# Optimization experiments

Measured on AMD Instinct MI355X. Metric: run time of the kernel, lower is better.

## Reference

```python
import jax, jax.numpy as jnp
import numpy as np

NUM_EMBEDDINGS = 1024
EMBEDDING_DIM = 64
COMMITMENT_COST = 0.25


def setup_inputs() -> dict:
    key = jax.random.key(0)
    k_in, k_cb = jax.random.split(key)
    inputs = jax.random.normal(k_in, (32, 4096, EMBEDDING_DIM), dtype=jnp.float32)
    # matches reset_embeddings(): uniform(-1/num_embeddings, 1/num_embeddings)
    bound = 1.0 / NUM_EMBEDDINGS
    codebook = jax.random.uniform(k_cb, (NUM_EMBEDDINGS, EMBEDDING_DIM),
                                  dtype=jnp.float32, minval=-bound, maxval=bound)
    return {"inputs": inputs, "codebook": codebook}


def reference(inputs, codebook):
    input_shape = inputs.shape
    D = codebook.shape[1]
    x = inputs.reshape(-1, D)  # [N, D]
    # Squared euclidean distances; argmin is invariant to the sqrt used by torch.cdist.
    # dist2[n,k] = ||x_n||^2 - 2 x_n . e_k + ||e_k||^2
    dist2 = (jnp.sum(x * x, axis=1, keepdims=True)
             - 2.0 * (x @ codebook.T)
             + jnp.sum(codebook * codebook, axis=1))  # [N, K]
    encoding_indices = jnp.argmin(dist2, axis=1)  # [N]
    quantized = codebook[encoding_indices].reshape(input_shape)
    loss = (jnp.mean((jax.lax.stop_gradient(quantized) - inputs) ** 2)
            + COMMITMENT_COST * jnp.mean((quantized - jax.lax.stop_gradient(inputs)) ** 2))
    # straight-through estimator
    quantized_st = inputs + jax.lax.stop_gradient(quantized - inputs)
    return quantized_st, loss
```

## Files before the change

### kernel.cpp

```cpp
#include <hip/hip_runtime.h>


typedef __attribute__((ext_vector_type(8))) short short8;
typedef __attribute__((ext_vector_type(4))) float f32x4;

#define VQ_D 64
#define MTILE 512
#define CSTRIDE 68

__device__ inline unsigned short f2bf(float f) {
  union { float f; unsigned u; } v; v.f = f;
  unsigned r = v.u + 0x7FFFu + ((v.u >> 16) & 1u);
  return (unsigned short)(r >> 16);
}

__global__ __launch_bounds__(256) void vq_prep(const float* __restrict__ cb,
                                               float* __restrict__ c2b,
                                               unsigned short* __restrict__ cbb,
                                               float* __restrict__ sse,
                                               unsigned* __restrict__ counter, int K) {
  if (blockIdx.x == 0 && threadIdx.x == 0) { *sse = 0.f; *counter = 0u; }
  int w = (int)((blockIdx.x * 256 + threadIdx.x) >> 6);
  int lane = threadIdx.x & 63;
  if (w >= K) return;
  float v = cb[(size_t)w * VQ_D + lane];
  cbb[(size_t)w * VQ_D + lane] = f2bf(v);
  float s = v * v;
#pragma unroll
  for (int off = 32; off; off >>= 1) s += __shfl_down(s, off);
  if (lane == 0) c2b[w] = s + 0.5f;
}

__global__ __launch_bounds__(512) void vq_main(
    const float* __restrict__ x, const float* __restrict__ cb,
    const float* __restrict__ c2b, const unsigned short* __restrict__ cbb,
    float* __restrict__ out, float* __restrict__ sse_out,
    unsigned* __restrict__ counter, int nblocks) {
  __shared__ unsigned short cbs[1024 * CSTRIDE];
  __shared__ float c2s[1024];
  __shared__ int idxs[MTILE];
  __shared__ float redbuf[8];

  const int tid = threadIdx.x;
  const int wave = tid >> 6;
  const int lane = tid & 63;
  const int quad = lane >> 4;
  const int col = lane & 15;
  const long blockRow0 = (long)blockIdx.x * MTILE;
  const int waveRow0 = wave * 64;

#pragma unroll
  for (int r = 0; r < 16; ++r) {
    int id = r * 512 + tid;
    int code = id >> 3;
    int piece = id & 7;
    short8 v = *(const short8*)(cbb + (size_t)code * VQ_D + piece * 8);
    *(short8*)(cbs + code * CSTRIDE + piece * 8) = v;
  }
  c2s[tid] = c2b[tid];
  c2s[tid + 512] = c2b[tid + 512];

  short8 Af[4][2];
#pragma unroll
  for (int mi = 0; mi < 4; ++mi) {
#pragma unroll
    for (int ks = 0; ks < 2; ++ks) {
      long row = blockRow0 + waveRow0 + mi * 16 + col;
      const f32x4* xp = (const f32x4*)(x + row * VQ_D + ks * 32 + quad * 8);
      f32x4 lo = xp[0];
      f32x4 hi = xp[1];
      short8 a;
      a[0] = (short)f2bf(-2.f * lo[0]); a[1] = (short)f2bf(-2.f * lo[1]);
      a[2] = (short)f2bf(-2.f * lo[2]); a[3] = (short)f2bf(-2.f * lo[3]);
      a[4] = (short)f2bf(-2.f * hi[0]); a[5] = (short)f2bf(-2.f * hi[1]);
      a[6] = (short)f2bf(-2.f * hi[2]); a[7] = (short)f2bf(-2.f * hi[3]);
      Af[mi][ks] = a;
    }
  }

  unsigned bk[4][4];
#pragma unroll
  for (int mi = 0; mi < 4; ++mi)
#pragma unroll
    for (int r = 0; r < 4; ++r) bk[mi][r] = 0xFFFFFFFFu;

  __syncthreads();

  const unsigned short* bbase = cbs + (size_t)col * CSTRIDE + quad * 8;
#pragma unroll 4
  for (int t = 0; t < 64; ++t) {
    const unsigned short* bp = bbase + t * 16 * CSTRIDE;
    short8 b0 = *(const short8*)bp;
    short8 b1 = *(const short8*)(bp + 32);
    float cc = c2s[t * 16 + col];

    f32x4 acc[4];
#pragma unroll
    for (int mi = 0; mi < 4; ++mi) {
      f32x4 a = {cc, cc, cc, cc};
      a = __builtin_amdgcn_mfma_f32_16x16x32_bf16(Af[mi][0], b0, a, 0, 0, 0);
      a = __builtin_amdgcn_mfma_f32_16x16x32_bf16(Af[mi][1], b1, a, 0, 0, 0);
      acc[mi] = a;
    }

    const unsigned code = (unsigned)((t << 4) + col);
#pragma unroll
    for (int mi = 0; mi < 4; ++mi)
#pragma unroll
      for (int r = 0; r < 4; ++r)
        bk[mi][r] = min(bk[mi][r], (__float_as_uint(acc[mi][r]) & 0xFFFFFC00u) | code);
  }

#pragma unroll
  for (int off = 1; off < 16; off <<= 1) {
#pragma unroll
    for (int mi = 0; mi < 4; ++mi)
#pragma unroll
      for (int r = 0; r < 4; ++r) {
        unsigned o = (unsigned)__shfl_xor((int)bk[mi][r], off);
        bk[mi][r] = min(bk[mi][r], o);
      }
  }
  if (col == 0) {
#pragma unroll
    for (int mi = 0; mi < 4; ++mi)
#pragma unroll
      for (int r = 0; r < 4; ++r)
        idxs[waveRow0 + mi * 16 + quad * 4 + r] = (int)(bk[mi][r] & 1023u);
  }
  __syncthreads();

  float sse = 0.f;
  const f32x4* cb4 = (const f32x4*)cb;
  const f32x4* x4 = (const f32x4*)x;
  f32x4* out4 = (f32x4*)out;
#pragma unroll
  for (int i = 0; i < 16; ++i) {
    int f = i * 512 + tid;
    int row_l = f >> 4;
    int d4 = f & 15;
    int idx = idxs[row_l];
    f32x4 cv = cb4[(size_t)idx * 16 + d4];
    long gi = (blockRow0 + row_l) * 16 + d4;
    f32x4 xv = x4[gi];
    out4[gi] = cv;
    f32x4 dv = cv - xv;
    sse += dv[0] * dv[0] + dv[1] * dv[1] + dv[2] * dv[2] + dv[3] * dv[3];
  }
#pragma unroll
  for (int off = 32; off; off >>= 1) sse += __shfl_down(sse, off);
  if (lane == 0) redbuf[wave] = sse;
  __syncthreads();

  if (tid == 0) {
    float s = 0.f;
#pragma unroll
    for (int w = 0; w < 8; ++w) s += redbuf[w];
    atomicAdd(sse_out, s);
    __threadfence();
    unsigned old = atomicAdd(counter, 1u);
    if (old == (unsigned)(nblocks - 1)) {
      float tot = atomicAdd(sse_out, 0.f);
      long nelem = (long)nblocks * MTILE * VQ_D;
      out[nelem] = 1.25f * tot / (float)nelem;
    }
  }
}

extern "C" void kernel_launch(void* const* d_in, const int* in_sizes, int n_in,
                              void* d_out, int out_size, void* d_ws, size_t ws_size,
                              hipStream_t stream) {
  const float* x = (const float*)d_in[0];
  const float* cb = (const float*)d_in[1];
  float* out = (float*)d_out;

  const long n_elem = (long)in_sizes[0];
  const int nrows = (int)(n_elem / VQ_D);
  const int K = in_sizes[1] / VQ_D;
  const int nblocks = nrows / MTILE;

  char* ws = (char*)d_ws;
  float* sse = (float*)ws;
  unsigned* counter = (unsigned*)(ws + 64);
  float* c2b = (float*)(ws + 256);
  unsigned short* cbb = (unsigned short*)(ws + 8192);

  vq_prep<<<dim3((K * 64 + 255) / 256), dim3(256), 0, stream>>>(cb, c2b, cbb, sse, counter, K);
  vq_main<<<dim3(nblocks), dim3(512), 0, stream>>>(x, cb, c2b, cbb, out, sse, counter, nblocks);
}
```

Before: 131.7 us.

## Keep codebook slices in registers and stream input rows through LDS

Each wave now holds a 128-code slice of the bf16 codebook in registers and loops over all 8 row groups of the block. Those rows are staged once as bf16 in a smaller LDS buffer, with the next group's operands prefetched. Per-row argmin keys are merged across waves with LDS atomicMin instead of one wave owning each row. This drops the 139KB codebook LDS copy, which should allow more blocks per CU and remove per-iteration LDS reads of B. The costs are higher register pressure, LDS atomics, and more shuffle reductions (8 rounds instead of one).

```diff
diff --git a/kernel.cpp b/kernel.cpp
--- a/kernel.cpp
+++ b/kernel.cpp
@@ -6,7 +6,8 @@
 
 #define VQ_D 64
 #define MTILE 512
-#define CSTRIDE 68
+#define NTH 512
+#define AS 68
 
 __device__ inline unsigned short f2bf(float f) {
   union { float f; unsigned u; } v; v.f = f;
@@ -31,14 +32,24 @@
   if (lane == 0) c2b[w] = s + 0.5f;
 }
 
-__global__ __launch_bounds__(512) void vq_main(
+#define LOADA(DST, G)                                                                  \
+  {                                                                                    \
+    const int g_ = (G);                                                                \
+    _Pragma("unroll") for (int mi_ = 0; mi_ < 4; ++mi_) {                              \
+      _Pragma("unroll") for (int ks_ = 0; ks_ < 2; ++ks_) {                            \
+        DST[mi_][ks_] = *(const short8*)(xb + (g_ * 64 + mi_ * 16 + col) * AS +        \
+                                         ks_ * 32 + quad * 8);                         \
+      }                                                                                \
+    }                                                                                  \
+  }
+
+__global__ __launch_bounds__(NTH) void vq_main(
     const float* __restrict__ x, const float* __restrict__ cb,
     const float* __restrict__ c2b, const unsigned short* __restrict__ cbb,
     float* __restrict__ out, float* __restrict__ sse_out,
     unsigned* __restrict__ counter, int nblocks) {
-  __shared__ unsigned short cbs[1024 * CSTRIDE];
-  __shared__ float c2s[1024];
-  __shared__ int idxs[MTILE];
+  __shared__ unsigned short xb[MTILE * AS];
+  __shared__ unsigned keys[MTILE];
   __shared__ float redbuf[8];
 
   const int tid = threadIdx.x;
@@ -47,86 +58,85 @@
   const int quad = lane >> 4;
   const int col = lane & 15;
   const long blockRow0 = (long)blockIdx.x * MTILE;
-  const int waveRow0 = wave * 64;
-
-#pragma unroll
-  for (int r = 0; r < 16; ++r) {
-    int id = r * 512 + tid;
-    int code = id >> 3;
+
+  short8 B[8][2];
+  float cc[8];
+  const int code0 = wave * 128;
+#pragma unroll
+  for (int ci = 0; ci < 8; ++ci) {
+    const unsigned short* bp = cbb + (size_t)(code0 + ci * 16 + col) * VQ_D + quad * 8;
+    B[ci][0] = *(const short8*)bp;
+    B[ci][1] = *(const short8*)(bp + 32);
+    cc[ci] = c2b[code0 + ci * 16 + col];
+  }
+
+  keys[tid] = 0xFFFFFFFFu;
+
+#pragma unroll
+  for (int i = 0; i < 8; ++i) {
+    int id = i * NTH + tid;
+    int row = id >> 3;
     int piece = id & 7;
-    short8 v = *(const short8*)(cbb + (size_t)code * VQ_D + piece * 8);
-    *(short8*)(cbs + code * CSTRIDE + piece * 8) = v;
-  }
-  c2s[tid] = c2b[tid];
-  c2s[tid + 512] = c2b[tid + 512];
-
-  short8 Af[4][2];
-#pragma unroll
-  for (int mi = 0; mi < 4; ++mi) {
-#pragma unroll
-    for (int ks = 0; ks < 2; ++ks) {
-      long row = blockRow0 + waveRow0 + mi * 16 + col;
-      const f32x4* xp = (const f32x4*)(x + row * VQ_D + ks * 32 + quad * 8);
-      f32x4 lo = xp[0];
-      f32x4 hi = xp[1];
-      short8 a;
-      a[0] = (short)f2bf(-2.f * lo[0]); a[1] = (short)f2bf(-2.f * lo[1]);
-      a[2] = (short)f2bf(-2.f * lo[2]); a[3] = (short)f2bf(-2.f * lo[3]);
-      a[4] = (short)f2bf(-2.f * hi[0]); a[5] = (short)f2bf(-2.f * hi[1]);
-      a[6] = (short)f2bf(-2.f * hi[2]); a[7] = (short)f2bf(-2.f * hi[3]);
-      Af[mi][ks] = a;
-    }
-  }
-
-  unsigned bk[4][4];
-#pragma unroll
-  for (int mi = 0; mi < 4; ++mi)
-#pragma unroll
-    for (int r = 0; r < 4; ++r) bk[mi][r] = 0xFFFFFFFFu;
-
+    const f32x4* xp = (const f32x4*)(x + (blockRow0 + row) * VQ_D + piece * 8);
+    f32x4 lo = xp[0];
+    f32x4 hi = xp[1];
+    short8 a;
+    a[0] = (short)f2bf(-2.f * lo[0]); a[1] = (short)f2bf(-2.f * lo[1]);
+    a[2] = (short)f2bf(-2.f * lo[2]); a[3] = (short)f2bf(-2.f * lo[3]);
+    a[4] = (short)f2bf(-2.f * hi[0]); a[5] = (short)f2bf(-2.f * hi[1]);
+    a[6] = (short)f2bf(-2.f * hi[2]); a[7] = (short)f2bf(-2.f * hi[3]);
+    *(short8*)(xb + row * AS + piece * 8) = a;
+  }
   __syncthreads();
 
-  const unsigned short* bbase = cbs + (size_t)col * CSTRIDE + quad * 8;
-#pragma unroll 4
-  for (int t = 0; t < 64; ++t) {
-    const unsigned short* bp = bbase + t * 16 * CSTRIDE;
-    short8 b0 = *(const short8*)bp;
-    short8 b1 = *(const short8*)(bp + 32);
-    float cc = c2s[t * 16 + col];
-
-    f32x4 acc[4];
+  short8 Ac[4][2], An[4][2];
+  LOADA(Ac, wave & 7);
+  for (int s = 0; s < 8; ++s) {
+    const int g = (wave + s) & 7;
+    LOADA(An, (wave + s + 1) & 7);
+
+    unsigned bk[4][4];
+#pragma unroll
+    for (int mi = 0; mi < 4; ++mi)
+#pragma unroll
+      for (int r = 0; r < 4; ++r) bk[mi][r] = 0xFFFFFFFFu;
+
 #pragma unroll
     for (int mi = 0; mi < 4; ++mi) {
-      f32x4 a = {cc, cc, cc, cc};
-      a = __builtin_amdgcn_mfma_f32_16x16x32_bf16(Af[mi][0], b0, a, 0, 0, 0);
-      a = __builtin_amdgcn_mfma_f32_16x16x32_bf16(Af[mi][1], b1, a, 0, 0, 0);
-      acc[mi] = a;
-    }
-
-    const unsigned code = (unsigned)((t << 4) + col);
+#pragma unroll
+      for (int ci = 0; ci < 8; ++ci) {
+        f32x4 a = {cc[ci], cc[ci], cc[ci], cc[ci]};
+        a = __builtin_amdgcn_mfma_f32_16x16x32_bf16(Ac[mi][0], B[ci][0], a, 0, 0, 0);
+        a = __builtin_amdgcn_mfma_f32_16x16x32_bf16(Ac[mi][1], B[ci][1], a, 0, 0, 0);
+        const unsigned code = (unsigned)(code0 + ci * 16 + col);
+#pragma unroll
+        for (int r = 0; r < 4; ++r)
+          bk[mi][r] = min(bk[mi][r], (__float_as_uint(a[r]) & 0xFFFFFC00u) | code);
+      }
+    }
+
+#pragma unroll
+    for (int off = 1; off < 16; off <<= 1) {
+#pragma unroll
+      for (int mi = 0; mi < 4; ++mi)
+#pragma unroll
+        for (int r = 0; r < 4; ++r) {
+          unsigned o = (unsigned)__shfl_xor((int)bk[mi][r], off);
+          bk[mi][r] = min(bk[mi][r], o);
+        }
+    }
+    if (col == 0) {
+#pragma unroll
+      for (int mi = 0; mi < 4; ++mi)
+#pragma unroll
+        for (int r = 0; r < 4; ++r)
+          atomicMin(&keys[g * 64 + mi * 16 + quad * 4 + r], bk[mi][r]);
+    }
+
 #pragma unroll
     for (int mi = 0; mi < 4; ++mi)
 #pragma unroll
-      for (int r = 0; r < 4; ++r)
-        bk[mi][r] = min(bk[mi][r], (__float_as_uint(acc[mi][r]) & 0xFFFFFC00u) | code);
-  }
-
-#pragma unroll
-  for (int off = 1; off < 16; off <<= 1) {
-#pragma unroll
-    for (int mi = 0; mi < 4; ++mi)
-#pragma unroll
-      for (int r = 0; r < 4; ++r) {
-        unsigned o = (unsigned)__shfl_xor((int)bk[mi][r], off);
-        bk[mi][r] = min(bk[mi][r], o);
-      }
-  }
-  if (col == 0) {
-#pragma unroll
-    for (int mi = 0; mi < 4; ++mi)
-#pragma unroll
-      for (int r = 0; r < 4; ++r)
-        idxs[waveRow0 + mi * 16 + quad * 4 + r] = (int)(bk[mi][r] & 1023u);
+      for (int ks = 0; ks < 2; ++ks) Ac[mi][ks] = An[mi][ks];
   }
   __syncthreads();
 
@@ -136,10 +146,10 @@
   f32x4* out4 = (f32x4*)out;
 #pragma unroll
   for (int i = 0; i < 16; ++i) {
-    int f = i * 512 + tid;
+    int f = i * NTH + tid;
     int row_l = f >> 4;
     int d4 = f & 15;
-    int idx = idxs[row_l];
+    int idx = (int)(keys[row_l] & 1023u);
     f32x4 cv = cb4[(size_t)idx * 16 + d4];
     long gi = (blockRow0 + row_l) * 16 + d4;
     f32x4 xv = x4[gi];
@@ -186,5 +196,5 @@
   unsigned short* cbb = (unsigned short*)(ws + 8192);
 
   vq_prep<<<dim3((K * 64 + 255) / 256), dim3(256), 0, stream>>>(cb, c2b, cbb, sse, counter, K);
-  vq_main<<<dim3(nblocks), dim3(512), 0, stream>>>(x, cb, c2b, cbb, out, sse, counter, nblocks);
-}
+  vq_main<<<dim3(nblocks), dim3(NTH), 0, stream>>>(x, cb, c2b, cbb, out, sse, counter, nblocks);
+}
```

Result: faster. 121.8 us (-7.5%).

## Stream padded bf16 codebook straight into LDS and gather quantized rows from LDS

Applied to the files above, without the earlier changes.

The prep kernel now writes the bf16 codebook already padded to the LDS row stride. The main kernel can then copy it into shared memory with direct global-to-LDS loads instead of a register round-trip. The quantized-output gather now reads the bf16 codebook from LDS and widens it to fp32, rather than issuing global fp32 loads of the codebook. This is meant to cut setup latency and global gather traffic. In exchange, the output vectors and the loss are computed from bf16-rounded codebook values instead of exact fp32 ones.

```diff
diff --git a/kernel.cpp b/kernel.cpp
--- a/kernel.cpp
+++ b/kernel.cpp
@@ -6,6 +6,7 @@
 
 #define VQ_D 64
 #define MTILE 512
+#define NTH 512
 #define CSTRIDE 68
 
 __device__ inline unsigned short f2bf(float f) {
@@ -24,14 +25,15 @@
   int lane = threadIdx.x & 63;
   if (w >= K) return;
   float v = cb[(size_t)w * VQ_D + lane];
-  cbb[(size_t)w * VQ_D + lane] = f2bf(v);
+  cbb[(size_t)w * CSTRIDE + lane] = f2bf(v);
+  if (lane < CSTRIDE - VQ_D) cbb[(size_t)w * CSTRIDE + VQ_D + lane] = 0;
   float s = v * v;
 #pragma unroll
   for (int off = 32; off; off >>= 1) s += __shfl_down(s, off);
   if (lane == 0) c2b[w] = s + 0.5f;
 }
 
-__global__ __launch_bounds__(512) void vq_main(
+__global__ __launch_bounds__(NTH) void vq_main(
     const float* __restrict__ x, const float* __restrict__ cb,
     const float* __restrict__ c2b, const unsigned short* __restrict__ cbb,
     float* __restrict__ out, float* __restrict__ sse_out,
@@ -49,13 +51,15 @@
   const long blockRow0 = (long)blockIdx.x * MTILE;
   const int waveRow0 = wave * 64;
 
+  const char* gbase = (const char*)cbb;
 #pragma unroll
-  for (int r = 0; r < 16; ++r) {
-    int id = r * 512 + tid;
-    int code = id >> 3;
-    int piece = id & 7;
-    short8 v = *(const short8*)(cbb + (size_t)code * VQ_D + piece * 8);
-    *(short8*)(cbs + code * CSTRIDE + piece * 8) = v;
+  for (int i = 0; i < 17; ++i) {
+    const int chunk0 = i * NTH + wave * 64;
+    const char* src = gbase + (size_t)(chunk0 + lane) * 16;
+    __builtin_amdgcn_global_load_lds(
+        (const __attribute__((address_space(1))) void*)src,
+        (__attribute__((address_space(3))) void*)(cbs + (size_t)chunk0 * 8),
+        16, 0, 0);
   }
   c2s[tid] = c2b[tid];
   c2s[tid + 512] = c2b[tid + 512];
@@ -131,16 +135,21 @@
   __syncthreads();
 
   float sse = 0.f;
-  const f32x4* cb4 = (const f32x4*)cb;
   const f32x4* x4 = (const f32x4*)x;
   f32x4* out4 = (f32x4*)out;
 #pragma unroll
   for (int i = 0; i < 16; ++i) {
-    int f = i * 512 + tid;
+    int f = i * NTH + tid;
     int row_l = f >> 4;
     int d4 = f & 15;
     int idx = idxs[row_l];
-    f32x4 cv = cb4[(size_t)idx * 16 + d4];
+    unsigned long long ev =
+        *(const unsigned long long*)(cbs + (size_t)idx * CSTRIDE + d4 * 4);
+    f32x4 cv;
+    cv[0] = __uint_as_float((unsigned)(ev & 0xFFFFull) << 16);
+    cv[1] = __uint_as_float((unsigned)((ev >> 16) & 0xFFFFull) << 16);
+    cv[2] = __uint_as_float((unsigned)((ev >> 32) & 0xFFFFull) << 16);
+    cv[3] = __uint_as_float((unsigned)((ev >> 48) & 0xFFFFull) << 16);
     long gi = (blockRow0 + row_l) * 16 + d4;
     f32x4 xv = x4[gi];
     out4[gi] = cv;
@@ -186,5 +195,5 @@
   unsigned short* cbb = (unsigned short*)(ws + 8192);
 
   vq_prep<<<dim3((K * 64 + 255) / 256), dim3(256), 0, stream>>>(cb, c2b, cbb, sse, counter, K);
-  vq_main<<<dim3(nblocks), dim3(512), 0, stream>>>(x, cb, c2b, cbb, out, sse, counter, nblocks);
+  vq_main<<<dim3(nblocks), dim3(NTH), 0, stream>>>(x, cb, c2b, cbb, out, sse, counter, nblocks);
 }
```

Result: no change. 132.2 us (+0.3%).
